# Kernel optimization log

Hardware: AMD Instinct MI355X
Metric: run time of the kernel (lower is better)

The kernel has to match this reference:

```python
import jax, jax.numpy as jnp
import numpy as np

EMBED_DIM = 768
NUM_HEADS = 12
MAX_LEN = 512
BATCH = 8
SEQ = 512
HEAD_DIM = EMBED_DIM // NUM_HEADS


def setup_inputs() -> dict:
    key = jax.random.key(0)
    ks = jax.random.split(key, 7)
    x = jax.random.normal(ks[0], (BATCH, SEQ, EMBED_DIM), dtype=jnp.float32)
    mask = jnp.ones((BATCH, SEQ), dtype=jnp.int32)
    Wq = jax.random.normal(ks[1], (EMBED_DIM, EMBED_DIM), dtype=jnp.float32) * (1.0 / np.sqrt(EMBED_DIM))
    Wk = jax.random.normal(ks[2], (EMBED_DIM, EMBED_DIM), dtype=jnp.float32) * (1.0 / np.sqrt(EMBED_DIM))
    Wv = jax.random.normal(ks[3], (EMBED_DIM, EMBED_DIM), dtype=jnp.float32) * (1.0 / np.sqrt(EMBED_DIM))
    rel_pos = jax.random.normal(ks[4], (2 * MAX_LEN - 1, NUM_HEADS), dtype=jnp.float32)
    Wo = jax.random.normal(ks[5], (EMBED_DIM, EMBED_DIM), dtype=jnp.float32) * (1.0 / np.sqrt(EMBED_DIM))
    bo = jax.random.normal(ks[6], (EMBED_DIM,), dtype=jnp.float32) * 0.02
    return {"x": x, "mask": mask, "Wq": Wq, "Wk": Wk, "Wv": Wv,
            "rel_pos": rel_pos, "Wo": Wo, "bo": bo}


def reference(x, mask, Wq, Wk, Wv, rel_pos, Wo, bo):
    B, S, E = x.shape
    H, D = NUM_HEADS, HEAD_DIM
    Q = (x @ Wq).reshape(B, S, H, D)
    K = (x @ Wk).reshape(B, S, H, D)
    V = (x @ Wv).reshape(B, S, H, D)
    # scores: [B, H, S, S]
    scores = jnp.einsum('bqhd,bkhd->bhqk', Q, K) / np.sqrt(D).astype(np.float32)
    # relative position bias: idx[q,k] = k - q + max_len - 1, clamped
    pos = jnp.arange(S)
    idx = jnp.clip(pos[None, :] - pos[:, None] + MAX_LEN - 1, 0, 2 * MAX_LEN - 2)
    bias = rel_pos[idx]                       # [S, S, H]
    scores = scores + jnp.transpose(bias, (2, 0, 1))[None]  # [1,H,S,S]
    # mask: b i * b j -> [B,1,S,S]
    m2 = (mask[:, None, :, None] * mask[:, None, None, :]) != 0
    mask_value = -jnp.finfo(scores.dtype).max
    scores = jnp.where(m2, scores, mask_value)
    attn = jax.nn.softmax(scores, axis=-1)
    out = jnp.einsum('bhqk,bkhd->bqhd', attn, V).reshape(B, S, E)
    out = out @ Wo + bo  # dropout is identity in eval mode
    return out
```

## Files before the change

kernel.cpp:

```cpp
#include <hip/hip_runtime.h>
#include <hip/hip_bf16.h>
#include <cfloat>
#include <cstdint>
#include <cmath>

#define EMBED 768
#define NHEAD 12
#define SEQB  8
#define SEQ   512
#define HDIM  64
#define WMAT  589824

typedef __attribute__((ext_vector_type(8))) short short8;
typedef __attribute__((ext_vector_type(4))) short short4v;
typedef __attribute__((ext_vector_type(4))) float f32x4;

__device__ __forceinline__ short f2bf(float f) {
  uint32_t u = __float_as_uint(f);
  u += 0x7FFF + ((u >> 16) & 1u);
  return (short)(u >> 16);
}

__device__ __forceinline__ void gload_lds16(const void* g, void* l) {
  __builtin_amdgcn_global_load_lds((const __attribute__((address_space(1))) void*)g,
                                   (__attribute__((address_space(3))) void*)l, 16, 0, 0);
}

__global__ void k_cast_x(const float* __restrict__ x, short* __restrict__ xb) {
  int i = blockIdx.x * blockDim.x + threadIdx.x;
  const int n4 = SEQB * SEQ * EMBED / 4;
  if (i < n4) {
    float4 v = ((const float4*)x)[i];
    short4v o;
    o.x = f2bf(v.x); o.y = f2bf(v.y); o.z = f2bf(v.z); o.w = f2bf(v.w);
    ((short4v*)xb)[i] = o;
  }
}

__global__ void k_cast_wt(const float* __restrict__ Wq, const float* __restrict__ Wk,
                          const float* __restrict__ Wv, const float* __restrict__ Wo,
                          short* __restrict__ Wt) {
  __shared__ float tile[32][33];
  const int mat = blockIdx.z;
  const float* src = (mat == 0) ? Wq : (mat == 1) ? Wk : (mat == 2) ? Wv : Wo;
  const int n0 = blockIdx.x * 32, k0 = blockIdx.y * 32;
  const int tx = threadIdx.x & 31, ty = threadIdx.x >> 5;
  #pragma unroll
  for (int rr = 0; rr < 4; rr++)
    tile[ty + rr * 8][tx] = src[(size_t)(k0 + ty + rr * 8) * EMBED + n0 + tx];
  __syncthreads();
  short* dst = Wt + (size_t)mat * WMAT;
  #pragma unroll
  for (int rr = 0; rr < 4; rr++)
    dst[(size_t)(n0 + ty + rr * 8) * EMBED + k0 + tx] = f2bf(tile[tx][ty + rr * 8]);
}

template <int MODE>
__launch_bounds__(256)
__global__ void k_gemm(const short* __restrict__ A, const short* __restrict__ B,
                       short* __restrict__ O0, short* __restrict__ O1,
                       short* __restrict__ O2,
                       float* __restrict__ OF, const float* __restrict__ bias) {
  __shared__ __attribute__((aligned(16))) short As[128 * 32];
  __shared__ __attribute__((aligned(16))) short Bs[128 * 32];
  const int tid = threadIdx.x;
  const int lane = tid & 63, w = tid >> 6;
  const int g = lane >> 4, c = lane & 15;
  const int wi = (w >> 1) * 64, wj = (w & 1) * 64;
  const int i0 = blockIdx.y * 128, j0 = blockIdx.x * 128;

  f32x4 acc[4][4];
  #pragma unroll
  for (int a = 0; a < 4; a++)
    #pragma unroll
    for (int b2 = 0; b2 < 4; b2++) acc[a][b2] = (f32x4){0.f, 0.f, 0.f, 0.f};

  for (int k0 = 0; k0 < EMBED; k0 += 32) {
    if (k0) __syncthreads();
    #pragma unroll
    for (int it = 0; it < 2; it++) {
      int gi = tid + it * 256;
      int row = gi >> 2, q = gi & 3;
      gload_lds16(A + (size_t)(i0 + row) * EMBED + k0 + q * 8, As + gi * 8);
      gload_lds16(B + (size_t)(j0 + row) * EMBED + k0 + q * 8, Bs + gi * 8);
    }
    __syncthreads();
    short8 aF[4], bF[4];
    #pragma unroll
    for (int mi = 0; mi < 4; mi++) aF[mi] = *(const short8*)&As[(wi + mi * 16 + c) * 32 + g * 8];
    #pragma unroll
    for (int nj = 0; nj < 4; nj++) bF[nj] = *(const short8*)&Bs[(wj + nj * 16 + c) * 32 + g * 8];
    #pragma unroll
    for (int mi = 0; mi < 4; mi++)
      #pragma unroll
      for (int nj = 0; nj < 4; nj++)
        acc[mi][nj] = __builtin_amdgcn_mfma_f32_16x16x32_bf16(aF[mi], bF[nj], acc[mi][nj], 0, 0, 0);
  }

  #pragma unroll
  for (int mi = 0; mi < 4; mi++) {
    int i = i0 + wi + mi * 16 + 4 * g;
    #pragma unroll
    for (int nj = 0; nj < 4; nj++) {
      int j = j0 + wj + nj * 16 + c;
      f32x4 v = acc[mi][nj];
      if (MODE == 0) {
        int n = i, m = j;
        int b = m >> 9, s = m & 511;
        if (n < 1536) {
          short* dst = O0; int nn = n;
          if (n >= 768) { dst = O1; nn -= 768; }
          int h = nn >> 6, d = nn & 63;
          short4v o; o.x = f2bf(v.x); o.y = f2bf(v.y); o.z = f2bf(v.z); o.w = f2bf(v.w);
          *(short4v*)&dst[(size_t)(((b * 12 + h) * 512 + s) * 64 + d)] = o;
        } else {
          int nn = n - 1536;
          int h = nn >> 6, d = nn & 63;
          size_t base = ((size_t)(b * 12 + h) * 64 + d) * 512 + s;
          O2[base] = f2bf(v.x); O2[base + 512] = f2bf(v.y);
          O2[base + 1024] = f2bf(v.z); O2[base + 1536] = f2bf(v.w);
        }
      } else {
        int n = i, m = j;
        float4 bb = *(const float4*)&bias[n];
        float4 o; o.x = v.x + bb.x; o.y = v.y + bb.y; o.z = v.z + bb.z; o.w = v.w + bb.w;
        *(float4*)&OF[(size_t)m * EMBED + n] = o;
      }
    }
  }
}

__launch_bounds__(256)
__global__ void k_attn(const short* __restrict__ Q, const short* __restrict__ K,
                       const short* __restrict__ Vt, const int* __restrict__ mask,
                       const float* __restrict__ rel_pos, short* __restrict__ attO) {
  __shared__ float bias_lds[1024];
  __shared__ int mask_lds[512];
  __shared__ __attribute__((aligned(16))) short Plds[4][16 * 32];
  const int tid = threadIdx.x;
  const int lane = tid & 63, w = tid >> 6;
  const int g = lane >> 4, c = lane & 15;
  const int bid = blockIdx.x;
  const int q0 = (bid / 96) * 64;
  const int bh = bid % 96;
  const int b = bh / 12, h = bh % 12;
  const short* Qb = Q + (size_t)bh * (512 * 64);
  const short* Kb = K + (size_t)bh * (512 * 64);
  const short* Vb = Vt + (size_t)bh * (64 * 512);

  for (int i = tid; i < 1023; i += 256) bias_lds[i] = rel_pos[i * 12 + h] - 16.0f;
  for (int i = tid; i < 512; i += 256) mask_lds[i] = mask[b * 512 + i];
  __syncthreads();

  short8 qf[2];
  #pragma unroll
  for (int dc = 0; dc < 2; dc++)
    qf[dc] = *(const short8*)&Qb[(q0 + w * 16 + c) * 64 + dc * 32 + g * 8];

  int qrow[4], mq[4], bbase[4];
  #pragma unroll
  for (int r = 0; r < 4; r++) {
    qrow[r] = q0 + w * 16 + 4 * g + r;
    mq[r] = mask_lds[qrow[r]];
    bbase[r] = 511 - qrow[r];
  }

  float l_part[4];
  f32x4 accO[4];
  #pragma unroll
  for (int r = 0; r < 4; r++) l_part[r] = 0.f;
  #pragma unroll
  for (int dt = 0; dt < 4; dt++) accO[dt] = (f32x4){0.f, 0.f, 0.f, 0.f};

  short8 kf[4], vf[4], nkf[4], nvf[4];
  #define LOADKV(K0, KK, VV)                                                        \
    {                                                                               \
      _Pragma("unroll")                                                             \
      for (int ct = 0; ct < 2; ct++)                                                \
        _Pragma("unroll")                                                           \
        for (int dc = 0; dc < 2; dc++)                                              \
          KK[ct * 2 + dc] = *(const short8*)&Kb[((K0) + ct * 16 + c) * 64 + dc * 32 + g * 8]; \
      _Pragma("unroll")                                                             \
      for (int dt = 0; dt < 4; dt++)                                                \
        VV[dt] = *(const short8*)&Vb[(dt * 16 + c) * 512 + (K0) + g * 8];           \
    }
  LOADKV(0, kf, vf);

  short* Pw = &Plds[w][0];
  const int rdoff = c * 32 + ((g * 8) ^ (((c >> 2) & 3) << 3));

  for (int k0 = 0; k0 < 512; k0 += 32) {
    if (k0 + 32 < 512) LOADKV(k0 + 32, nkf, nvf);
    float p[2][4];
    #pragma unroll
    for (int ct = 0; ct < 2; ct++) {
      f32x4 s = (f32x4){0.f, 0.f, 0.f, 0.f};
      s = __builtin_amdgcn_mfma_f32_16x16x32_bf16(qf[0], kf[ct * 2 + 0], s, 0, 0, 0);
      s = __builtin_amdgcn_mfma_f32_16x16x32_bf16(qf[1], kf[ct * 2 + 1], s, 0, 0, 0);
      int krow = k0 + ct * 16 + c;
      int mk = mask_lds[krow];
      #pragma unroll
      for (int r = 0; r < 4; r++) {
        float arg = fmaf(s[r], 0.125f, bias_lds[krow + bbase[r]]);
        float pv = __expf(arg);
        if ((mq[r] & mk) == 0) pv = 0.f;
        p[ct][r] = pv;
        l_part[r] += pv;
      }
    }
    #pragma unroll
    for (int ct = 0; ct < 2; ct++)
      #pragma unroll
      for (int r = 0; r < 4; r++)
        Pw[(4 * g + r) * 32 + ((ct * 16 + c) ^ (g << 3))] = f2bf(p[ct][r]);
    short8 pa = *(const short8*)&Pw[rdoff];
    #pragma unroll
    for (int dt = 0; dt < 4; dt++)
      accO[dt] = __builtin_amdgcn_mfma_f32_16x16x32_bf16(pa, vf[dt], accO[dt], 0, 0, 0);
    #pragma unroll
    for (int i = 0; i < 4; i++) { kf[i] = nkf[i]; vf[i] = nvf[i]; }
  }

  float inv[4];
  #pragma unroll
  for (int r = 0; r < 4; r++) {
    float lr = l_part[r];
    #pragma unroll
    for (int off = 1; off < 16; off <<= 1) lr += __shfl_xor(lr, off);
    inv[r] = 1.0f / lr;
  }
  #pragma unroll
  for (int dt = 0; dt < 4; dt++)
    #pragma unroll
    for (int r = 0; r < 4; r++)
      attO[(size_t)(b * 512 + qrow[r]) * EMBED + h * 64 + dt * 16 + c] =
          f2bf(accO[dt][r] * inv[r]);
}

extern "C" void kernel_launch(void* const* d_in, const int* in_sizes, int n_in,
                              void* d_out, int out_size, void* d_ws, size_t ws_size,
                              hipStream_t stream) {
  const float* x = (const float*)d_in[0];
  const int* mask = (const int*)d_in[1];
  const float* Wq = (const float*)d_in[2];
  const float* Wk = (const float*)d_in[3];
  const float* Wv = (const float*)d_in[4];
  const float* rel_pos = (const float*)d_in[5];
  const float* Wo = (const float*)d_in[6];
  const float* bo = (const float*)d_in[7];
  float* out = (float*)d_out;

  char* ws = (char*)d_ws;
  short* xb = (short*)ws;
  short* Wt = (short*)(ws + 6291456);
  short* Qg = (short*)(ws + 6291456 + 4718592);
  short* Kg = Qg + 3145728;
  short* Vt = Kg + 3145728;
  short* attO = xb;

  k_cast_x<<<3072, 256, 0, stream>>>(x, xb);
  k_cast_wt<<<dim3(24, 24, 4), 256, 0, stream>>>(Wq, Wk, Wv, Wo, Wt);
  k_gemm<0><<<dim3(32, 18), 256, 0, stream>>>(Wt, xb, Qg, Kg, Vt, nullptr, nullptr);
  k_attn<<<768, 256, 0, stream>>>(Qg, Kg, Vt, mask, rel_pos, attO);
  k_gemm<2><<<dim3(32, 6), 256, 0, stream>>>(Wt + 3 * WMAT, attO, nullptr, nullptr, nullptr, out, bo);
}
```

Measured before the change: 176.8 us.

## Software-pipeline attention loop with double-buffered P tile and exp2 softmax

Restructures the attention inner loop into a fully unrolled, software-pipelined schedule. The PV MFMA for tile T-1 overlaps the QK MFMA and softmax for tile T, using double-buffered per-wave P LDS tiles and ping-pong K/V registers. It also folds log2(e) into the bias and scale so it can use exp2f, and replaces the manual bf16 rounding with the v_cvt_pk_bf16_f32 instruction. The LDS swizzle on P is removed, which may add bank conflicts, and the full unroll raises register pressure.

Result: no change. 178.7 us (+1.1%).

```diff
diff --git a/kernel.cpp b/kernel.cpp
--- a/kernel.cpp
+++ b/kernel.cpp
@@ -19,6 +19,12 @@
   uint32_t u = __float_as_uint(f);
   u += 0x7FFF + ((u >> 16) & 1u);
   return (short)(u >> 16);
+}
+
+__device__ __forceinline__ short f2bf1(float f) {
+  int r;
+  asm("v_cvt_pk_bf16_f32 %0, %1, %2" : "=v"(r) : "v"(f), "v"(f));
+  return (short)r;
 }
 
 __device__ __forceinline__ void gload_lds16(const void* g, void* l) {
@@ -136,7 +142,7 @@
                        const float* __restrict__ rel_pos, short* __restrict__ attO) {
   __shared__ float bias_lds[1024];
   __shared__ int mask_lds[512];
-  __shared__ __attribute__((aligned(16))) short Plds[4][16 * 32];
+  __shared__ __attribute__((aligned(16))) short Plds[4][2][16 * 32];
   const int tid = threadIdx.x;
   const int lane = tid & 63, w = tid >> 6;
   const int g = lane >> 4, c = lane & 15;
@@ -148,7 +154,8 @@
   const short* Kb = K + (size_t)bh * (512 * 64);
   const short* Vb = Vt + (size_t)bh * (64 * 512);
 
-  for (int i = tid; i < 1023; i += 256) bias_lds[i] = rel_pos[i * 12 + h] - 16.0f;
+  const float LOG2E = 1.44269504089f;
+  for (int i = tid; i < 1023; i += 256) bias_lds[i] = (rel_pos[i * 12 + h] - 16.0f) * LOG2E;
   for (int i = tid; i < 512; i += 256) mask_lds[i] = mask[b * 512 + i];
   __syncthreads();
 
@@ -172,53 +179,94 @@
   #pragma unroll
   for (int dt = 0; dt < 4; dt++) accO[dt] = (f32x4){0.f, 0.f, 0.f, 0.f};
 
-  short8 kf[4], vf[4], nkf[4], nvf[4];
-  #define LOADKV(K0, KK, VV)                                                        \
-    {                                                                               \
-      _Pragma("unroll")                                                             \
-      for (int ct = 0; ct < 2; ct++)                                                \
-        _Pragma("unroll")                                                           \
-        for (int dc = 0; dc < 2; dc++)                                              \
-          KK[ct * 2 + dc] = *(const short8*)&Kb[((K0) + ct * 16 + c) * 64 + dc * 32 + g * 8]; \
-      _Pragma("unroll")                                                             \
-      for (int dt = 0; dt < 4; dt++)                                                \
-        VV[dt] = *(const short8*)&Vb[(dt * 16 + c) * 512 + (K0) + g * 8];           \
+  short8 kf0[4], kf1[4], vf0[4], vf1[4];
+  const float SC = 0.125f * 1.44269504089f;
+
+  #define LOADK(K0, KK)                                                              \
+    { _Pragma("unroll")                                                              \
+      for (int ct = 0; ct < 2; ct++)                                                 \
+        _Pragma("unroll")                                                            \
+        for (int dc = 0; dc < 2; dc++)                                               \
+          KK[ct * 2 + dc] = *(const short8*)&Kb[((K0) + ct * 16 + c) * 64 + dc * 32 + g * 8]; }
+  #define LOADV(K0, VV)                                                              \
+    { _Pragma("unroll")                                                              \
+      for (int dt = 0; dt < 4; dt++)                                                 \
+        VV[dt] = *(const short8*)&Vb[(dt * 16 + c) * 512 + (K0) + g * 8]; }
+
+  #define SOFTMAX(T, KC, PDST)                                                       \
+    f32x4 s0 = (f32x4){0.f, 0.f, 0.f, 0.f}, s1 = s0;                                 \
+    s0 = __builtin_amdgcn_mfma_f32_16x16x32_bf16(qf[0], KC[0], s0, 0, 0, 0);         \
+    s0 = __builtin_amdgcn_mfma_f32_16x16x32_bf16(qf[1], KC[1], s0, 0, 0, 0);         \
+    s1 = __builtin_amdgcn_mfma_f32_16x16x32_bf16(qf[0], KC[2], s1, 0, 0, 0);         \
+    s1 = __builtin_amdgcn_mfma_f32_16x16x32_bf16(qf[1], KC[3], s1, 0, 0, 0);         \
+    {                                                                                \
+      const int krow = (T) * 32 + c;                                                 \
+      const int mk0 = mask_lds[krow], mk1 = mask_lds[krow + 16];                     \
+      _Pragma("unroll")                                                              \
+      for (int r = 0; r < 4; r++) {                                                  \
+        float a0 = fmaf(s0[r], SC, bias_lds[krow + bbase[r]]);                       \
+        float a1 = fmaf(s1[r], SC, bias_lds[krow + 16 + bbase[r]]);                  \
+        float p0 = exp2f(a0), p1 = exp2f(a1);                                        \
+        if ((mq[r] & mk0) == 0) p0 = 0.f;                                            \
+        if ((mq[r] & mk1) == 0) p1 = 0.f;                                            \
+        PDST[0][r] = p0; PDST[1][r] = p1;                                            \
+        l_part[r] += p0 + p1;                                                        \
+      }                                                                              \
     }
-  LOADKV(0, kf, vf);
-
-  short* Pw = &Plds[w][0];
-  const int rdoff = c * 32 + ((g * 8) ^ (((c >> 2) & 3) << 3));
-
-  for (int k0 = 0; k0 < 512; k0 += 32) {
-    if (k0 + 32 < 512) LOADKV(k0 + 32, nkf, nvf);
-    float p[2][4];
-    #pragma unroll
-    for (int ct = 0; ct < 2; ct++) {
-      f32x4 s = (f32x4){0.f, 0.f, 0.f, 0.f};
-      s = __builtin_amdgcn_mfma_f32_16x16x32_bf16(qf[0], kf[ct * 2 + 0], s, 0, 0, 0);
-      s = __builtin_amdgcn_mfma_f32_16x16x32_bf16(qf[1], kf[ct * 2 + 1], s, 0, 0, 0);
-      int krow = k0 + ct * 16 + c;
-      int mk = mask_lds[krow];
-      #pragma unroll
-      for (int r = 0; r < 4; r++) {
-        float arg = fmaf(s[r], 0.125f, bias_lds[krow + bbase[r]]);
-        float pv = __expf(arg);
-        if ((mq[r] & mk) == 0) pv = 0.f;
-        p[ct][r] = pv;
-        l_part[r] += pv;
-      }
-    }
-    #pragma unroll
-    for (int ct = 0; ct < 2; ct++)
-      #pragma unroll
-      for (int r = 0; r < 4; r++)
-        Pw[(4 * g + r) * 32 + ((ct * 16 + c) ^ (g << 3))] = f2bf(p[ct][r]);
-    short8 pa = *(const short8*)&Pw[rdoff];
+
+  #define WRITEP(PW, PSRC)                                                           \
+    { _Pragma("unroll")                                                              \
+      for (int ct = 0; ct < 2; ct++)                                                 \
+        _Pragma("unroll")                                                            \
+        for (int r = 0; r < 4; r++)                                                  \
+          (PW)[(4 * g + r) * 32 + ct * 16 + c] = f2bf1(PSRC[ct][r]); }
+
+  short* Pb0 = &Plds[w][0][0];
+  short* Pb1 = &Plds[w][1][0];
+  const int rdoff = c * 32 + g * 8;
+
+  LOADK(0, kf0); LOADV(0, vf0);
+  {
+    float p_[2][4];
+    SOFTMAX(0, kf0, p_)
+    LOADK(32, kf1); LOADV(32, vf1);
+    WRITEP(Pb0, p_)
+  }
+
+  #define ATTN_ITER(T, KC, KN, VP, PW, PR)                                           \
+  {                                                                                  \
+    short8 pa = *(const short8*)&(PR)[rdoff];                                        \
+    float p_[2][4];                                                                  \
+    SOFTMAX(T, KC, p_)                                                               \
+    if ((T) < 15) LOADK(((T) + 1) * 32, KN);                                         \
+    _Pragma("unroll")                                                                \
+    for (int dt = 0; dt < 4; dt++)                                                   \
+      accO[dt] = __builtin_amdgcn_mfma_f32_16x16x32_bf16(pa, VP[dt], accO[dt], 0, 0, 0); \
+    if ((T) < 15) LOADV(((T) + 1) * 32, VP);                                         \
+    WRITEP(PW, p_)                                                                   \
+  }
+
+  ATTN_ITER(1,  kf1, kf0, vf0, Pb1, Pb0)
+  ATTN_ITER(2,  kf0, kf1, vf1, Pb0, Pb1)
+  ATTN_ITER(3,  kf1, kf0, vf0, Pb1, Pb0)
+  ATTN_ITER(4,  kf0, kf1, vf1, Pb0, Pb1)
+  ATTN_ITER(5,  kf1, kf0, vf0, Pb1, Pb0)
+  ATTN_ITER(6,  kf0, kf1, vf1, Pb0, Pb1)
+  ATTN_ITER(7,  kf1, kf0, vf0, Pb1, Pb0)
+  ATTN_ITER(8,  kf0, kf1, vf1, Pb0, Pb1)
+  ATTN_ITER(9,  kf1, kf0, vf0, Pb1, Pb0)
+  ATTN_ITER(10, kf0, kf1, vf1, Pb0, Pb1)
+  ATTN_ITER(11, kf1, kf0, vf0, Pb1, Pb0)
+  ATTN_ITER(12, kf0, kf1, vf1, Pb0, Pb1)
+  ATTN_ITER(13, kf1, kf0, vf0, Pb1, Pb0)
+  ATTN_ITER(14, kf0, kf1, vf1, Pb0, Pb1)
+  ATTN_ITER(15, kf1, kf0, vf0, Pb1, Pb0)
+
+  {
+    short8 pa = *(const short8*)&Pb1[rdoff];
     #pragma unroll
     for (int dt = 0; dt < 4; dt++)
-      accO[dt] = __builtin_amdgcn_mfma_f32_16x16x32_bf16(pa, vf[dt], accO[dt], 0, 0, 0);
-    #pragma unroll
-    for (int i = 0; i < 4; i++) { kf[i] = nkf[i]; vf[i] = nvf[i]; }
+      accO[dt] = __builtin_amdgcn_mfma_f32_16x16x32_bf16(pa, vf1[dt], accO[dt], 0, 0, 0);
   }
 
   float inv[4];
```

## Stage K/V tiles through double-buffered swizzled LDS via async global_load_lds

Applied to the files above, without the earlier changes.

The attention kernel now loads each 32-key K/V tile once per block into double-buffered LDS using global_load_lds with XOR swizzles. Previously each of the four waves loaded its own copy from global memory into registers. Each wave reads its MFMA fragments from LDS, and a block barrier per iteration protects buffer reuse. The softmax is rewritten to use exp2f with log2e folded into the bias and scale, and bf16 conversion now uses the hardware v_cvt_pk_bf16_f32 instruction. The P write swizzle is also removed, which may introduce LDS bank conflicts.

Measured after the change: 153.8 us. 13.0% less time.

```diff
diff --git a/kernel.cpp b/kernel.cpp
--- a/kernel.cpp
+++ b/kernel.cpp
@@ -19,6 +19,12 @@
   uint32_t u = __float_as_uint(f);
   u += 0x7FFF + ((u >> 16) & 1u);
   return (short)(u >> 16);
+}
+
+__device__ __forceinline__ short f2bf1(float f) {
+  int r;
+  asm("v_cvt_pk_bf16_f32 %0, %1, %2" : "=v"(r) : "v"(f), "v"(f));
+  return (short)r;
 }
 
 __device__ __forceinline__ void gload_lds16(const void* g, void* l) {
@@ -137,6 +143,8 @@
   __shared__ float bias_lds[1024];
   __shared__ int mask_lds[512];
   __shared__ __attribute__((aligned(16))) short Plds[4][16 * 32];
+  __shared__ __attribute__((aligned(16))) short Kbuf[2][32 * 64];
+  __shared__ __attribute__((aligned(16))) short Vbuf[2][64 * 32];
   const int tid = threadIdx.x;
   const int lane = tid & 63, w = tid >> 6;
   const int g = lane >> 4, c = lane & 15;
@@ -148,14 +156,28 @@
   const short* Kb = K + (size_t)bh * (512 * 64);
   const short* Vb = Vt + (size_t)bh * (64 * 512);
 
-  for (int i = tid; i < 1023; i += 256) bias_lds[i] = rel_pos[i * 12 + h] - 16.0f;
+  const float LOG2E = 1.44269504089f;
+  for (int i = tid; i < 1023; i += 256) bias_lds[i] = (rel_pos[i * 12 + h] - 16.0f) * LOG2E;
   for (int i = tid; i < 512; i += 256) mask_lds[i] = mask[b * 512 + i];
-  __syncthreads();
+
+  const int krow_s = tid >> 3, kc_s = tid & 7;
+  const int vrow_s = tid >> 2, vc_s = tid & 3;
+  #define STAGEKV(T, BUF)                                                             \
+    {                                                                                 \
+      gload_lds16(Kb + ((T) * 32 + krow_s) * 64 + (kc_s ^ (krow_s & 7)) * 8,          \
+                  &Kbuf[BUF][tid * 8]);                                               \
+      gload_lds16(Vb + (size_t)vrow_s * 512 + (T) * 32 + (vc_s ^ ((vrow_s >> 1) & 3)) * 8, \
+                  &Vbuf[BUF][tid * 8]);                                               \
+    }
+
+  STAGEKV(0, 0)
 
   short8 qf[2];
   #pragma unroll
   for (int dc = 0; dc < 2; dc++)
     qf[dc] = *(const short8*)&Qb[(q0 + w * 16 + c) * 64 + dc * 32 + g * 8];
+
+  __syncthreads();
 
   int qrow[4], mq[4], bbase[4];
   #pragma unroll
@@ -172,53 +194,61 @@
   #pragma unroll
   for (int dt = 0; dt < 4; dt++) accO[dt] = (f32x4){0.f, 0.f, 0.f, 0.f};
 
-  short8 kf[4], vf[4], nkf[4], nvf[4];
-  #define LOADKV(K0, KK, VV)                                                        \
-    {                                                                               \
-      _Pragma("unroll")                                                             \
-      for (int ct = 0; ct < 2; ct++)                                                \
-        _Pragma("unroll")                                                           \
-        for (int dc = 0; dc < 2; dc++)                                              \
-          KK[ct * 2 + dc] = *(const short8*)&Kb[((K0) + ct * 16 + c) * 64 + dc * 32 + g * 8]; \
-      _Pragma("unroll")                                                             \
-      for (int dt = 0; dt < 4; dt++)                                                \
-        VV[dt] = *(const short8*)&Vb[(dt * 16 + c) * 512 + (K0) + g * 8];           \
-    }
-  LOADKV(0, kf, vf);
-
+  const float SC = 0.125f * 1.44269504089f;
   short* Pw = &Plds[w][0];
-  const int rdoff = c * 32 + ((g * 8) ^ (((c >> 2) & 3) << 3));
-
-  for (int k0 = 0; k0 < 512; k0 += 32) {
-    if (k0 + 32 < 512) LOADKV(k0 + 32, nkf, nvf);
-    float p[2][4];
-    #pragma unroll
-    for (int ct = 0; ct < 2; ct++) {
-      f32x4 s = (f32x4){0.f, 0.f, 0.f, 0.f};
-      s = __builtin_amdgcn_mfma_f32_16x16x32_bf16(qf[0], kf[ct * 2 + 0], s, 0, 0, 0);
-      s = __builtin_amdgcn_mfma_f32_16x16x32_bf16(qf[1], kf[ct * 2 + 1], s, 0, 0, 0);
-      int krow = k0 + ct * 16 + c;
-      int mk = mask_lds[krow];
+  const int rdoff = c * 32 + g * 8;
+  const int kswz = c & 7;
+  const int vswz = (c >> 1) & 3;
+
+  int bufsel = 0;
+  for (int t = 0; t < 16; ++t) {
+    if (t < 15) STAGEKV(t + 1, bufsel ^ 1)
+    const short* Kt = &Kbuf[bufsel][0];
+    const short* Vs = &Vbuf[bufsel][0];
+
+    short8 kf[4], vf[4];
+    #pragma unroll
+    for (int ct = 0; ct < 2; ct++)
+      #pragma unroll
+      for (int dc = 0; dc < 2; dc++)
+        kf[ct * 2 + dc] = *(const short8*)&Kt[(ct * 16 + c) * 64 + ((dc * 4 + g) ^ kswz) * 8];
+    #pragma unroll
+    for (int dt = 0; dt < 4; dt++)
+      vf[dt] = *(const short8*)&Vs[(dt * 16 + c) * 32 + ((g ^ vswz)) * 8];
+
+    f32x4 s0 = (f32x4){0.f, 0.f, 0.f, 0.f}, s1 = s0;
+    s0 = __builtin_amdgcn_mfma_f32_16x16x32_bf16(qf[0], kf[0], s0, 0, 0, 0);
+    s0 = __builtin_amdgcn_mfma_f32_16x16x32_bf16(qf[1], kf[1], s0, 0, 0, 0);
+    s1 = __builtin_amdgcn_mfma_f32_16x16x32_bf16(qf[0], kf[2], s1, 0, 0, 0);
+    s1 = __builtin_amdgcn_mfma_f32_16x16x32_bf16(qf[1], kf[3], s1, 0, 0, 0);
+
+    float p_[2][4];
+    {
+      const int krow = t * 32 + c;
+      const int mk0 = mask_lds[krow], mk1 = mask_lds[krow + 16];
       #pragma unroll
       for (int r = 0; r < 4; r++) {
-        float arg = fmaf(s[r], 0.125f, bias_lds[krow + bbase[r]]);
-        float pv = __expf(arg);
-        if ((mq[r] & mk) == 0) pv = 0.f;
-        p[ct][r] = pv;
-        l_part[r] += pv;
+        float a0 = fmaf(s0[r], SC, bias_lds[krow + bbase[r]]);
+        float a1 = fmaf(s1[r], SC, bias_lds[krow + 16 + bbase[r]]);
+        float p0 = exp2f(a0), p1 = exp2f(a1);
+        if ((mq[r] & mk0) == 0) p0 = 0.f;
+        if ((mq[r] & mk1) == 0) p1 = 0.f;
+        p_[0][r] = p0; p_[1][r] = p1;
+        l_part[r] += p0 + p1;
       }
     }
     #pragma unroll
     for (int ct = 0; ct < 2; ct++)
       #pragma unroll
       for (int r = 0; r < 4; r++)
-        Pw[(4 * g + r) * 32 + ((ct * 16 + c) ^ (g << 3))] = f2bf(p[ct][r]);
+        Pw[(4 * g + r) * 32 + ct * 16 + c] = f2bf1(p_[ct][r]);
     short8 pa = *(const short8*)&Pw[rdoff];
     #pragma unroll
     for (int dt = 0; dt < 4; dt++)
       accO[dt] = __builtin_amdgcn_mfma_f32_16x16x32_bf16(pa, vf[dt], accO[dt], 0, 0, 0);
-    #pragma unroll
-    for (int i = 0; i < 4; i++) { kf[i] = nkf[i]; vf[i] = nvf[i]; }
+
+    __syncthreads();
+    bufsel ^= 1;
   }
 
   float inv[4];
```
